# Kernel tuning notes

Hardware: AMD Instinct MI355X
Metric: run time of the kernel (lower is better)

Reference implementation:

```python
import jax, jax.numpy as jnp
import numpy as np

EPS_BN = 1e-5  # torch BatchNorm1d default eps


def setup_inputs() -> dict:
    key = jax.random.key(0)
    k1, k2, k3 = jax.random.split(key, 3)
    B, C, L = 512, 8, 16384
    attn_maps = jax.random.normal(k1, (B, C, L), dtype=jnp.float32)
    target_matrix = jax.random.uniform(k2, (B, C, C), dtype=jnp.float32)
    conv_bias = jnp.ones((C,), dtype=jnp.float32) * 0.5  # nn.Parameter(torch.ones(8)/2)
    w_fc = jax.random.normal(k3, (3, 1), dtype=jnp.float32) * 0.1
    b_fc = jnp.zeros((3,), dtype=jnp.float32)
    return {"attn_maps": attn_maps, "target_matrix": target_matrix,
            "conv_bias": conv_bias, "w_fc": w_fc, "b_fc": b_fc}


def reference(attn_maps, target_matrix, conv_bias, w_fc, b_fc):
    B, C, L = attn_maps.shape  # C == 8 (fixed by the grouped 1x1 conv)
    # (attn - mean of per-row means) * 100; rows are uniform length so this is the global mean
    x = (attn_maps - jnp.mean(attn_maps)) * 100.0
    # grouped conv1d, kernel 1, weight == 5: per-channel affine, then sigmoid / 5
    bin_maps = jax.nn.sigmoid(5.0 * x + conv_bias[None, :, None]) / 5.0  # (B, C, L)
    b5 = bin_maps * 5.0
    # vectorized triangular IoU: intersection / union over the length dim
    inter = jnp.einsum('bil,bjl->bij', b5, b5)                     # (B, C, C)
    union = L - jnp.einsum('bil,bjl->bij', 1.0 - b5, 1.0 - b5)      # (B, C, C)
    tril = jnp.tril(jnp.ones((C, C), dtype=bool))
    sim = jnp.where(tril, inter / union, 0.0)
    # rep_type 'abs': sum of |sim - 100*target| over the lower triangle (incl. diag)
    tm = target_matrix * 100.0
    st = jnp.sum(jnp.where(tril, jnp.abs(sim - tm), 0.0), axis=(1, 2))  # (B,)
    # BatchNorm1d(1, affine=False) in training mode: normalize over the batch
    mu = jnp.mean(st)
    var = jnp.var(st)  # biased variance, as torch BN uses for normalization
    st_n = (st - mu) * jax.lax.rsqrt(var + EPS_BN)                  # (B,)
    # final linear 1 -> 3 (original Linear(128,3) is shape-inconsistent; see notes)
    out = st_n[:, None] @ w_fc.T + b_fc                              # (B, 3)
    return out
```

## Files before the change

### kernel.cpp

```cpp
#include <hip/hip_runtime.h>
#include <math.h>

typedef float f32x4 __attribute__((ext_vector_type(4)));
typedef _Float16 f16x2 __attribute__((ext_vector_type(2)));

#define B_DIM 512
#define C_DIM 8
#define L_DIM 16384
#define NELEM (B_DIM * C_DIM * L_DIM)
#define LOG2E 1.4426950408889634f
#define KA (-500.0f * LOG2E)

#if __has_builtin(__builtin_amdgcn_exp2f)
#define EXP2F __builtin_amdgcn_exp2f
#else
#define EXP2F exp2f
#endif

#if __has_builtin(__builtin_amdgcn_fdot2)
#define HAVE_FDOT2 1
#else
#define HAVE_FDOT2 0
#endif

#define H_NODE 0.25
#define F_P 1.2840254166877414f
#define F_M 0.7788007830714049f

#define TRI(i, j) ((i) * ((i) + 1) / 2 + (j))

#define WS_GRAM_OFF 8192

__global__ __launch_bounds__(256) void k_main(const f32x4* __restrict__ in4,
                                              const float* __restrict__ bias,
                                              float* __restrict__ asum,
                                              float* __restrict__ gram_t) {
  const int tid = threadIdx.x;
  const int lane = tid & 63, wv = tid >> 6;
  const int nodesel = tid >> 7;
  const int pt = tid & 127;
  const int b = blockIdx.x;

  const float Fn = nodesel ? F_M : F_P;
  float kc[C_DIM];
#pragma unroll
  for (int c = 0; c < C_DIM; ++c) kc[c] = bias[c] * (-LOG2E);

  float acc[44];
#pragma unroll
  for (int k = 0; k < 44; ++k) acc[k] = 0.f;
  float asacc = 0.f;

#if HAVE_FDOT2
  const f16x2 ONE2 = {(_Float16)1.f, (_Float16)1.f};
#endif

  const f32x4* base = in4 + (size_t)b * (C_DIM * 4096) + pt;

  auto compute = [&](const f32x4* v) {
#pragma unroll
    for (int p = 0; p < 2; ++p) {
      float sx[C_DIM], sy[C_DIM];
#if HAVE_FDOT2
      f16x2 s2[C_DIM];
#endif
#pragma unroll
      for (int c = 0; c < C_DIM; ++c) {
        const float ax = p ? v[c].z : v[c].x;
        const float ay = p ? v[c].w : v[c].y;
        if (nodesel == 0) asacc += ax + ay;
        const float Ex = EXP2F(fmaf(KA, ax, kc[c]));
        const float Ey = EXP2F(fmaf(KA, ay, kc[c]));
        sx[c] = __builtin_amdgcn_rcpf(fmaf(Ex, Fn, 1.f));
        sy[c] = __builtin_amdgcn_rcpf(fmaf(Ey, Fn, 1.f));
#if HAVE_FDOT2
        s2[c] = __builtin_bit_cast(f16x2, __builtin_amdgcn_cvt_pkrtz(sx[c], sy[c]));
        acc[c] = __builtin_amdgcn_fdot2(s2[c], ONE2, acc[c], false);
#else
        acc[c] += sx[c] + sy[c];
#endif
      }
#pragma unroll
      for (int i = 0; i < C_DIM; ++i)
#pragma unroll
        for (int j = 0; j <= i; ++j) {
#if HAVE_FDOT2
          acc[8 + TRI(i, j)] =
              __builtin_amdgcn_fdot2(s2[i], s2[j], acc[8 + TRI(i, j)], false);
#else
          acc[8 + TRI(i, j)] =
              fmaf(sx[i], sx[j], fmaf(sy[i], sy[j], acc[8 + TRI(i, j)]));
#endif
        }
    }
  };

  f32x4 va[C_DIM], vb[C_DIM];
#pragma unroll
  for (int c = 0; c < C_DIM; ++c) va[c] = base[c * 4096];

#pragma unroll 1
  for (int it = 0; it < 32; it += 2) {
#pragma unroll
    for (int c = 0; c < C_DIM; ++c) vb[c] = base[c * 4096 + (it + 1) * 128];
    compute(va);
    if (it + 2 < 32) {
#pragma unroll
      for (int c = 0; c < C_DIM; ++c) va[c] = base[c * 4096 + (it + 2) * 128];
    }
    compute(vb);
  }

  __shared__ float lgr[4][44];
  __shared__ float las[2];
#pragma unroll
  for (int k = 0; k < 44; ++k) {
    float x = acc[k];
#pragma unroll
    for (int off = 32; off; off >>= 1) x += __shfl_xor(x, off, 64);
    if (lane == 0) lgr[wv][k] = x;
  }
  if (nodesel == 0) {
    float x = asacc;
#pragma unroll
    for (int off = 32; off; off >>= 1) x += __shfl_xor(x, off, 64);
    if (lane == 0) las[wv] = x;
  }
  __syncthreads();
  if (tid < 88) {
    const int n = tid / 44, k = tid - n * 44;
    gram_t[(size_t)(n * 44 + k) * 512 + b] = lgr[2 * n][k] + lgr[2 * n + 1][k];
  }
  if (tid == 96) asum[b] = las[0] + las[1];
}

__global__ __launch_bounds__(512) void k_final(const float* __restrict__ asum,
                                               const float* __restrict__ gram_t,
                                               const float* __restrict__ target,
                                               const float* __restrict__ w_fc,
                                               const float* __restrict__ b_fc,
                                               float* __restrict__ out) {
  const int t = threadIdx.x;
  __shared__ double red[512];

  red[t] = (double)asum[t];
  __syncthreads();
  for (int off = 256; off; off >>= 1) {
    if (t < off) red[t] += red[t + off];
    __syncthreads();
  }
  const double th = 500.0 * (red[0] / (double)NELEM);
  __syncthreads();

  const double w0 = (th + H_NODE) / (2.0 * H_NODE);
  const double w1 = (H_NODE - th) / (2.0 * H_NODE);

  const float* g = gram_t + t;
  double S[8], T[36];
#pragma unroll
  for (int i = 0; i < 8; ++i)
    S[i] = w0 * (double)g[(0 + i) * 512] + w1 * (double)g[(44 + i) * 512];
#pragma unroll
  for (int k = 0; k < 36; ++k)
    T[k] = w0 * (double)g[(8 + k) * 512] + w1 * (double)g[(52 + k) * 512];

  double st = 0.0;
#pragma unroll
  for (int i = 0; i < 8; ++i)
#pragma unroll
    for (int j = 0; j <= i; ++j) {
      double inter = T[TRI(i, j)];
      double uni = (S[i] + S[j]) - inter;
      double sim = inter / uni;
      double tm = 100.0 * (double)target[t * 64 + i * 8 + j];
      st += fabs(sim - tm);
    }

  red[t] = st;
  __syncthreads();
  for (int off = 256; off; off >>= 1) {
    if (t < off) red[t] += red[t + off];
    __syncthreads();
  }
  const double mean = red[0] * (1.0 / 512.0);
  __syncthreads();
  const double dd = st - mean;
  red[t] = dd * dd;
  __syncthreads();
  for (int off = 256; off; off >>= 1) {
    if (t < off) red[t] += red[t + off];
    __syncthreads();
  }
  const double var = red[0] * (1.0 / 512.0);
  const float stn = (float)((st - mean) / sqrt(var + 1e-5));
#pragma unroll
  for (int k = 0; k < 3; ++k)
    out[t * 3 + k] = fmaf(stn, w_fc[k], b_fc[k]);
}

extern "C" void kernel_launch(void* const* d_in, const int* in_sizes, int n_in,
                              void* d_out, int out_size, void* d_ws, size_t ws_size,
                              hipStream_t stream) {
  const float* attn   = (const float*)d_in[0];
  const float* target = (const float*)d_in[1];
  const float* bias   = (const float*)d_in[2];
  const float* w_fc   = (const float*)d_in[3];
  const float* b_fc   = (const float*)d_in[4];
  float* out = (float*)d_out;
  float* ws  = (float*)d_ws;

  float* asum   = ws;
  float* gram_t = ws + WS_GRAM_OFF;

  k_main<<<B_DIM, 256, 0, stream>>>((const f32x4*)attn, bias, asum, gram_t);
  k_final<<<1, 512, 0, stream>>>(asum, gram_t, target, w_fc, b_fc, out);
}
```

Baseline: 76.25 us.

## Split each batch row across two blocks with float2 loads and occupancy hint

Launches twice as many blocks, each covering half of a batch row's length using 8-byte float2 loads instead of 16-byte float4 loads. Partial gram sums and input sums for the two halves go to separate workspace slots, and the final kernel adds them. A launch_bounds minimum-blocks hint of 4 asks for lower register use and higher occupancy. The aim is to fill the GPU better, since 512 blocks cover only about two waves per CU on 256 CUs. The cost is narrower loads, possible register spills, and a little more work in the final kernel.

After: 86.81 us. 13.8% more time.

```diff
diff --git a/kernel.cpp b/kernel.cpp
--- a/kernel.cpp
+++ b/kernel.cpp
@@ -1,7 +1,7 @@
 #include <hip/hip_runtime.h>
 #include <math.h>
 
-typedef float f32x4 __attribute__((ext_vector_type(4)));
+typedef float f32x2 __attribute__((ext_vector_type(2)));
 typedef _Float16 f16x2 __attribute__((ext_vector_type(2)));
 
 #define B_DIM 512
@@ -31,15 +31,15 @@
 
 #define WS_GRAM_OFF 8192
 
-__global__ __launch_bounds__(256) void k_main(const f32x4* __restrict__ in4,
-                                              const float* __restrict__ bias,
-                                              float* __restrict__ asum,
-                                              float* __restrict__ gram_t) {
+__global__ __launch_bounds__(256, 4) void k_main(const f32x2* __restrict__ in2,
+                                                 const float* __restrict__ bias,
+                                                 float* __restrict__ asum,
+                                                 float* __restrict__ gram_t) {
   const int tid = threadIdx.x;
   const int lane = tid & 63, wv = tid >> 6;
   const int nodesel = tid >> 7;
   const int pt = tid & 127;
-  const int b = blockIdx.x;
+  const int b = blockIdx.x >> 1, half = blockIdx.x & 1;
 
   const float Fn = nodesel ? F_M : F_P;
   float kc[C_DIM];
@@ -55,61 +55,60 @@
   const f16x2 ONE2 = {(_Float16)1.f, (_Float16)1.f};
 #endif
 
-  const f32x4* base = in4 + (size_t)b * (C_DIM * 4096) + pt;
-
-  auto compute = [&](const f32x4* v) {
-#pragma unroll
-    for (int p = 0; p < 2; ++p) {
-      float sx[C_DIM], sy[C_DIM];
-#if HAVE_FDOT2
-      f16x2 s2[C_DIM];
-#endif
-#pragma unroll
-      for (int c = 0; c < C_DIM; ++c) {
-        const float ax = p ? v[c].z : v[c].x;
-        const float ay = p ? v[c].w : v[c].y;
-        if (nodesel == 0) asacc += ax + ay;
-        const float Ex = EXP2F(fmaf(KA, ax, kc[c]));
-        const float Ey = EXP2F(fmaf(KA, ay, kc[c]));
-        sx[c] = __builtin_amdgcn_rcpf(fmaf(Ex, Fn, 1.f));
-        sy[c] = __builtin_amdgcn_rcpf(fmaf(Ey, Fn, 1.f));
-#if HAVE_FDOT2
-        s2[c] = __builtin_bit_cast(f16x2, __builtin_amdgcn_cvt_pkrtz(sx[c], sy[c]));
-        acc[c] = __builtin_amdgcn_fdot2(s2[c], ONE2, acc[c], false);
-#else
-        acc[c] += sx[c] + sy[c];
+  const f32x2* base = in2 + (size_t)b * (C_DIM * 8192) + half * 4096 + pt;
+
+  auto compute = [&](const f32x2* v) {
+    float sx[C_DIM], sy[C_DIM];
+#if HAVE_FDOT2
+    f16x2 s2[C_DIM];
+#endif
+#pragma unroll
+    for (int c = 0; c < C_DIM; ++c) {
+      const float ax = v[c].x;
+      const float ay = v[c].y;
+      if (nodesel == 0) asacc += ax + ay;
+      const float Ex = EXP2F(fmaf(KA, ax, kc[c]));
+      const float Ey = EXP2F(fmaf(KA, ay, kc[c]));
+      sx[c] = __builtin_amdgcn_rcpf(fmaf(Ex, Fn, 1.f));
+      sy[c] = __builtin_amdgcn_rcpf(fmaf(Ey, Fn, 1.f));
+#if HAVE_FDOT2
+      s2[c] = __builtin_bit_cast(f16x2, __builtin_amdgcn_cvt_pkrtz(sx[c], sy[c]));
+      acc[c] = __builtin_amdgcn_fdot2(s2[c], ONE2, acc[c], false);
+#else
+      acc[c] += sx[c] + sy[c];
+#endif
+    }
+#pragma unroll
+    for (int i = 0; i < C_DIM; ++i)
+#pragma unroll
+      for (int j = 0; j <= i; ++j) {
+#if HAVE_FDOT2
+        acc[8 + TRI(i, j)] =
+            __builtin_amdgcn_fdot2(s2[i], s2[j], acc[8 + TRI(i, j)], false);
+#else
+        acc[8 + TRI(i, j)] =
+            fmaf(sx[i], sx[j], fmaf(sy[i], sy[j], acc[8 + TRI(i, j)]));
 #endif
       }
-#pragma unroll
-      for (int i = 0; i < C_DIM; ++i)
-#pragma unroll
-        for (int j = 0; j <= i; ++j) {
-#if HAVE_FDOT2
-          acc[8 + TRI(i, j)] =
-              __builtin_amdgcn_fdot2(s2[i], s2[j], acc[8 + TRI(i, j)], false);
-#else
-          acc[8 + TRI(i, j)] =
-              fmaf(sx[i], sx[j], fmaf(sy[i], sy[j], acc[8 + TRI(i, j)]));
-#endif
-        }
-    }
   };
 
-  f32x4 va[C_DIM], vb[C_DIM];
-#pragma unroll
-  for (int c = 0; c < C_DIM; ++c) va[c] = base[c * 4096];
+#define LOADBUF(dst, itx)                                                  \
+  do {                                                                     \
+    _Pragma("unroll") for (int c = 0; c < C_DIM; ++c)                      \
+        dst[c] = base[c * 8192 + (itx) * 128];                             \
+  } while (0)
+
+  f32x2 va[C_DIM], vb[C_DIM];
+  LOADBUF(va, 0);
 
 #pragma unroll 1
   for (int it = 0; it < 32; it += 2) {
-#pragma unroll
-    for (int c = 0; c < C_DIM; ++c) vb[c] = base[c * 4096 + (it + 1) * 128];
+    LOADBUF(vb, it + 1);
     compute(va);
-    if (it + 2 < 32) {
-#pragma unroll
-      for (int c = 0; c < C_DIM; ++c) va[c] = base[c * 4096 + (it + 2) * 128];
-    }
+    if (it + 2 < 32) LOADBUF(va, it + 2);
     compute(vb);
   }
+#undef LOADBUF
 
   __shared__ float lgr[4][44];
   __shared__ float las[2];
@@ -129,9 +128,10 @@
   __syncthreads();
   if (tid < 88) {
     const int n = tid / 44, k = tid - n * 44;
-    gram_t[(size_t)(n * 44 + k) * 512 + b] = lgr[2 * n][k] + lgr[2 * n + 1][k];
-  }
-  if (tid == 96) asum[b] = las[0] + las[1];
+    gram_t[(size_t)((half * 2 + n) * 44 + k) * 512 + b] =
+        lgr[2 * n][k] + lgr[2 * n + 1][k];
+  }
+  if (tid == 96) asum[blockIdx.x] = las[0] + las[1];
 }
 
 __global__ __launch_bounds__(512) void k_final(const float* __restrict__ asum,
@@ -143,7 +143,7 @@
   const int t = threadIdx.x;
   __shared__ double red[512];
 
-  red[t] = (double)asum[t];
+  red[t] = (double)asum[2 * t] + (double)asum[2 * t + 1];
   __syncthreads();
   for (int off = 256; off; off >>= 1) {
     if (t < off) red[t] += red[t + off];
@@ -155,14 +155,21 @@
   const double w0 = (th + H_NODE) / (2.0 * H_NODE);
   const double w1 = (H_NODE - th) / (2.0 * H_NODE);
 
-  const float* g = gram_t + t;
   double S[8], T[36];
 #pragma unroll
-  for (int i = 0; i < 8; ++i)
-    S[i] = w0 * (double)g[(0 + i) * 512] + w1 * (double)g[(44 + i) * 512];
-#pragma unroll
-  for (int k = 0; k < 36; ++k)
-    T[k] = w0 * (double)g[(8 + k) * 512] + w1 * (double)g[(52 + k) * 512];
+  for (int i = 0; i < 8; ++i) S[i] = 0.0;
+#pragma unroll
+  for (int k = 0; k < 36; ++k) T[k] = 0.0;
+#pragma unroll
+  for (int h = 0; h < 2; ++h) {
+    const float* g = gram_t + (size_t)(h * 2) * 44 * 512 + t;
+#pragma unroll
+    for (int i = 0; i < 8; ++i)
+      S[i] += w0 * (double)g[(0 + i) * 512] + w1 * (double)g[(44 + i) * 512];
+#pragma unroll
+    for (int k = 0; k < 36; ++k)
+      T[k] += w0 * (double)g[(8 + k) * 512] + w1 * (double)g[(52 + k) * 512];
+  }
 
   double st = 0.0;
 #pragma unroll
@@ -212,6 +219,6 @@
   float* asum   = ws;
   float* gram_t = ws + WS_GRAM_OFF;
 
-  k_main<<<B_DIM, 256, 0, stream>>>((const f32x4*)attn, bias, asum, gram_t);
+  k_main<<<B_DIM * 2, 256, 0, stream>>>((const f32x2*)attn, bias, asum, gram_t);
   k_final<<<1, 512, 0, stream>>>(asum, gram_t, target, w_fc, b_fc, out);
 }
```
